# Optimization experiments

Measured on AMD Instinct MI355X. Metric: run time of the kernel, lower is better.

The kernel has to match this reference:

```python
import jax, jax.numpy as jnp
import numpy as np

DK, DV, NH = 512, 256, 8  # matches init_kwargs


def rel_to_abs(x):
    # x: (B, N, L, 2L-1) -> (B, N, L, L) via pad/reshape trick
    B, N, L, _ = x.shape
    x = jnp.pad(x, ((0, 0), (0, 0), (0, 0), (0, 1)))          # (B,N,L,2L)
    x = x.reshape(B, N, L * 2 * L)
    x = jnp.pad(x, ((0, 0), (0, 0), (0, L - 1)))
    x = x.reshape(B, N, L + 1, 2 * L - 1)
    return x[:, :, :L, L - 1:]


def relative_logits_1d(q, rel_k):
    # q: (B, nh, A, Wd, dkh); rel_k: (dkh, 2*Wd-1)
    B, nh, A, Wd, _ = q.shape
    rel = jnp.einsum('bnawc,cm->bnawm', q, rel_k)             # (B,nh,A,Wd,2Wd-1)
    rel = rel.reshape(B, nh * A, Wd, 2 * Wd - 1)
    rel = rel_to_abs(rel).reshape(B, nh, A, 1, Wd, Wd)
    return jnp.broadcast_to(rel, (B, nh, A, A, Wd, Wd))


def reference(x, w_qkv, w_conv, w_out, key_rel_h, key_rel_w):
    B, Cin, H, W = x.shape
    dkh, dvh = DK // NH, DV // NH
    L = H * W
    # 1x1 qkv projection (stride 1)
    qkv = jnp.einsum('bchw,oc->bohw', x, w_qkv)               # (B, 2dk+dv, H, W)
    q = qkv[:, :DK]
    k = qkv[:, DK:2 * DK]
    v = qkv[:, 2 * DK:]
    flat_q = q.reshape(B, NH, dkh, L) * (dkh ** -0.5)
    flat_k = k.reshape(B, NH, dkh, L)
    flat_v = v.reshape(B, NH, dvh, L)
    logits = jnp.einsum('bncs,bnct->bnst', flat_q, flat_k)     # (B,nh,L,L)
    # relative position logits (uses the already-scaled q, as in the torch code)
    qr = flat_q.reshape(B, NH, dkh, H, W).transpose(0, 1, 3, 4, 2)  # (B,nh,H,W,dkh)
    w_rel = relative_logits_1d(qr, key_rel_w)                  # (B,nh,H,H,W,W)
    h_rel = relative_logits_1d(qr.transpose(0, 1, 3, 2, 4), key_rel_h)  # (B,nh,W,W,H,H)
    h_rel = h_rel.transpose(0, 1, 2, 4, 3, 5).reshape(B, NH, L, L)
    w_rel = w_rel.transpose(0, 1, 4, 2, 5, 3).reshape(B, NH, L, L)
    logits = logits + h_rel + w_rel
    weights = jax.nn.softmax(logits, axis=-1)
    attn = jnp.einsum('bnst,bnct->bnsc', weights, flat_v)      # (B,nh,L,dvh)
    attn = attn.transpose(0, 1, 3, 2).reshape(B, DV, H, W)
    attn = jnp.einsum('bchw,oc->bohw', attn, w_out)            # 1x1 out_proj
    conv_out = jax.lax.conv_general_dilated(
        x, w_conv, window_strides=(1, 1), padding=[(1, 1), (1, 1)],
        dimension_numbers=('NCHW', 'OIHW', 'NCHW'))            # (B, out_c-dv, H, W)
    return jnp.concatenate([conv_out, attn], axis=1)


def setup_inputs() -> dict:
    key = jax.random.key(0)
    ks = jax.random.split(key, 6)
    H, W, Cin = 32, 32, 256
    return {
        'x': jax.random.normal(ks[0], (8, Cin, H, W), jnp.float32),
        'w_qkv': jax.random.normal(ks[1], (2 * DK + DV, Cin), jnp.float32) * 0.02,
        'w_conv': jax.random.normal(ks[2], (256, Cin, 3, 3), jnp.float32) * 0.02,
        'w_out': jax.random.normal(ks[3], (DV, DV), jnp.float32) * 0.02,
        'key_rel_h': DK ** -0.5 + jax.random.normal(ks[4], (DK // NH, 2 * H - 1), jnp.float32),
        'key_rel_w': DK ** -0.5 + jax.random.normal(ks[5], (DK // NH, 2 * W - 1), jnp.float32),
    }
```

## Files before the change

kernel.cpp:

```cpp
#include <hip/hip_runtime.h>
#include <cstddef>
#include <cstdint>

#define NB 8
#define CIN 256
#define LL 1024
#define DKC 512
#define DVC 256
#define XPSTRIDE 295936

typedef short short8 __attribute__((ext_vector_type(8)));
typedef float f32x4 __attribute__((ext_vector_type(4)));

__device__ __forceinline__ unsigned short f2bf(float f) {
  unsigned int u = __float_as_uint(f);
  u += 0x7fffu + ((u >> 16) & 1u);
  return (unsigned short)(u >> 16);
}
__device__ __forceinline__ float bf2f(unsigned short u) {
  return __uint_as_float(((unsigned int)u) << 16);
}

__global__ __launch_bounds__(256) void prep_all(
    const float* __restrict__ x, const float* __restrict__ wconv,
    const float* __restrict__ wqkv, const float* __restrict__ wout,
    const float* __restrict__ krh, const float* __restrict__ krw,
    unsigned short* __restrict__ xTp, unsigned short* __restrict__ wtap,
    unsigned short* __restrict__ wqbf, unsigned short* __restrict__ woutbf,
    unsigned short* __restrict__ relTh, unsigned short* __restrict__ relTw) {
  __shared__ float tile[64][65];
  const int bx = blockIdx.x;
  const int tid = threadIdx.x;
  if (bx < 128) {
    const int st = bx & 15;
    const int b = bx >> 4;
    const int s0 = st * 64;
    const int h0 = st * 2;
    for (int cc = 0; cc < 4; ++cc) {
      const int c0 = cc * 64;
      {
        const int row = tid >> 2;
        const int j0 = (tid & 3) * 16;
#pragma unroll
        for (int k = 0; k < 4; ++k)
          *(float4*)&tile[row][j0 + k * 4] =
              *(const float4*)(x + ((size_t)(b * CIN + c0 + row)) * LL + s0 + j0 + k * 4);
      }
      __syncthreads();
      {
        const int sl = tid >> 2;
        const int cb = (tid & 3) * 16;
        unsigned short buf[16];
#pragma unroll
        for (int m = 0; m < 16; ++m) buf[m] = f2bf(tile[cb + m][sl]);
        const int hp = h0 + (sl >> 5) + 1;
        const int wp = (sl & 31) + 1;
        unsigned short* dst = xTp + (size_t)b * XPSTRIDE + (hp * 34 + wp) * 256 + c0 + cb;
        *(uint4*)dst = *(uint4*)&buf[0];
        *(uint4*)(dst + 8) = *(uint4*)&buf[8];
      }
      __syncthreads();
    }
  } else if (bx < 1184) {
    const int idx = (bx - 128) * 256 + tid;
    const int b = idx / 33792;
    const int rem = idx - b * 33792;
    const int pos = rem >> 8, c = rem & 255;
    int hp, wp;
    if (pos < 34) { hp = 0; wp = pos; }
    else if (pos < 68) { hp = 33; wp = pos - 34; }
    else if (pos < 100) { hp = pos - 68 + 1; wp = 0; }
    else { hp = pos - 100 + 1; wp = 33; }
    xTp[(size_t)b * XPSTRIDE + (hp * 34 + wp) * 256 + c] = 0;
  } else {
    const int idx = (bx - 1184) * 256 + tid;
    if (idx < 589824) {
      const int tap = idx >> 16;
      const int rem = idx & 65535;
      wtap[idx] = f2bf(wconv[(size_t)rem * 9 + tap]);
    } else if (idx < 917504) {
      const int j = idx - 589824;
      const int o = j >> 8;
      const float sc = (o < DKC) ? 0.125f * 1.44269504088896f : 1.0f;
      wqbf[j] = f2bf(wqkv[j] * sc);
    } else if (idx < 983040) {
      const int j = idx - 917504;
      woutbf[j] = f2bf(wout[j]);
    } else {
      const int j = idx - 983040;
      const int tbl = j >> 12;
      const int rest = j & 4095;
      const int m = rest >> 6, c = rest & 63;
      const float* src = tbl ? krw : krh;
      unsigned short* dst = tbl ? relTw : relTh;
      const float v = (m < 63) ? src[c * 63 + m] : 0.f;
      dst[m * 64 + c] = f2bf(v);
    }
  }
}

__global__ __launch_bounds__(256) void qkv_mfma(
    const unsigned short* __restrict__ xTp, const unsigned short* __restrict__ wqbf,
    unsigned short* __restrict__ qbf, unsigned short* __restrict__ kbf,
    unsigned short* __restrict__ vbf) {
  __shared__ __align__(16) char smem[16640];
  unsigned short* as = (unsigned short*)smem;
  unsigned short* bs = (unsigned short*)(smem + 8192);
  float (*trans)[65] = (float(*)[65])smem;

  const int tid = threadIdx.x;
  const int lane = tid & 63, w = tid >> 6;
  const int n16 = lane & 15, quad = lane >> 4;
  const int ot = blockIdx.x;
  const int st = blockIdx.y;
  const int b = blockIdx.z;
  const int o0 = ot * 64;
  const int s0 = st * 64;
  const int h0 = st * 2;
  const int trow = tid >> 3, ck = tid & 7;

  const unsigned short* xb = xTp + (size_t)b * XPSTRIDE;
  const unsigned short* wt = wqbf + (size_t)o0 * 256;
  const int wpos = (trow & 31) + 1;

  f32x4 acc[4];
#pragma unroll
  for (int nt = 0; nt < 4; ++nt) acc[nt] = (f32x4){0.f, 0.f, 0.f, 0.f};

  uint4 ra0, ra1, rb0, rb1;
  {
    ra0 = *(const uint4*)(wt + (size_t)trow * 256 + ck * 8);
    ra1 = *(const uint4*)(wt + (size_t)(trow + 32) * 256 + ck * 8);
    rb0 = *(const uint4*)(xb + (size_t)((h0 + 1) * 34 + wpos) * 256 + ck * 8);
    rb1 = *(const uint4*)(xb + (size_t)((h0 + 2) * 34 + wpos) * 256 + ck * 8);
  }
#pragma unroll
  for (int kc = 0; kc < 4; ++kc) {
    __syncthreads();
    *(uint4*)&as[trow * 64 + ((ck ^ (trow & 7)) * 8)] = ra0;
    *(uint4*)&as[(trow + 32) * 64 + ((ck ^ (trow & 7)) * 8)] = ra1;
    *(uint4*)&bs[trow * 64 + ((ck ^ (trow & 7)) * 8)] = rb0;
    *(uint4*)&bs[(trow + 32) * 64 + ((ck ^ (trow & 7)) * 8)] = rb1;
    __syncthreads();
    if (kc < 3) {
      const int c0 = (kc + 1) * 64;
      ra0 = *(const uint4*)(wt + (size_t)trow * 256 + c0 + ck * 8);
      ra1 = *(const uint4*)(wt + (size_t)(trow + 32) * 256 + c0 + ck * 8);
      rb0 = *(const uint4*)(xb + (size_t)((h0 + 1) * 34 + wpos) * 256 + c0 + ck * 8);
      rb1 = *(const uint4*)(xb + (size_t)((h0 + 2) * 34 + wpos) * 256 + c0 + ck * 8);
    }
    short8 a0 = *(const short8*)&as[(w * 16 + n16) * 64 + ((quad ^ (n16 & 7)) * 8)];
    short8 a1 = *(const short8*)&as[(w * 16 + n16) * 64 + (((quad + 4) ^ (n16 & 7)) * 8)];
#pragma unroll
    for (int nt = 0; nt < 4; ++nt) {
      short8 b0 = *(const short8*)&bs[(nt * 16 + n16) * 64 + ((quad ^ (n16 & 7)) * 8)];
      short8 b1 = *(const short8*)&bs[(nt * 16 + n16) * 64 + (((quad + 4) ^ (n16 & 7)) * 8)];
      acc[nt] = __builtin_amdgcn_mfma_f32_16x16x32_bf16(a0, b0, acc[nt], 0, 0, 0);
      acc[nt] = __builtin_amdgcn_mfma_f32_16x16x32_bf16(a1, b1, acc[nt], 0, 0, 0);
    }
  }
  __syncthreads();
#pragma unroll
  for (int nt = 0; nt < 4; ++nt)
#pragma unroll
    for (int reg = 0; reg < 4; ++reg)
      trans[w * 16 + quad * 4 + reg][nt * 16 + n16] = acc[nt][reg];
  __syncthreads();
  const int sl = tid >> 2;
  const int cseg = (tid & 3) * 16;
  unsigned short buf[16];
  if (ot < 16) {
#pragma unroll
    for (int m = 0; m < 16; ++m) buf[m] = f2bf(trans[cseg + m][sl]);
    unsigned short* dst;
    int head;
    if (ot < 8) { dst = qbf; head = ot; }
    else { dst = kbf; head = ot - 8; }
    const size_t base = (((size_t)(b * 8 + head)) * LL + s0 + sl) * 64 + cseg;
    *(uint4*)(dst + base) = *(uint4*)&buf[0];
    *(uint4*)(dst + base + 8) = *(uint4*)&buf[8];
  } else {
#pragma unroll
    for (int m = 0; m < 16; ++m) buf[m] = f2bf(trans[sl][cseg + m]);
    unsigned short* dst = vbf + ((size_t)b * DVC + (ot - 16) * 64 + sl) * LL + s0 + cseg;
    *(uint4*)dst = *(uint4*)&buf[0];
    *(uint4*)(dst + 8) = *(uint4*)&buf[8];
  }
}

__global__ __launch_bounds__(256) void conv_mfma(
    const unsigned short* __restrict__ xTp, const unsigned short* __restrict__ wtap,
    float* __restrict__ out) {
  __shared__ __align__(16) unsigned short as[2][64 * 64];
  __shared__ __align__(16) unsigned short bs[2][64 * 64];
  const int tid = threadIdx.x;
  const int lane = tid & 63, w = tid >> 6;
  const int n16 = lane & 15, quad = lane >> 4;
  const int ot = blockIdx.x;
  const int st = blockIdx.y;
  const int b = blockIdx.z;
  const int s0 = st * 64;
  const int h0 = st * 2;
  const int trow = tid >> 3;
  const int ck = tid & 7;

  const unsigned short* xb = xTp + (size_t)b * XPSTRIDE;
  const unsigned short* wbase = wtap + (size_t)(ot * 64) * 256;

  f32x4 acc[4];
#pragma unroll
  for (int nt = 0; nt < 4; ++nt) acc[nt] = (f32x4){0.f, 0.f, 0.f, 0.f};

  uint4 ra0, ra1, rb0, rb1;
  auto loadtile = [&](int it) {
    const int tap = it >> 2;
    const int c0 = (it & 3) * 64;
    const int dh = tap / 3 - 1;
    const int dw = tap - (tap / 3) * 3 - 1;
    const unsigned short* wt = wbase + (size_t)tap * 65536;
    ra0 = *(const uint4*)(wt + (size_t)trow * 256 + c0 + ck * 8);
    ra1 = *(const uint4*)(wt + (size_t)(trow + 32) * 256 + c0 + ck * 8);
    const int wp = (trow & 31) + dw + 1;
    rb0 = *(const uint4*)(xb + (size_t)((h0 + dh + 1) * 34 + wp) * 256 + c0 + ck * 8);
    rb1 = *(const uint4*)(xb + (size_t)((h0 + dh + 2) * 34 + wp) * 256 + c0 + ck * 8);
  };
  auto stage = [&](int bufi) {
    *(uint4*)&as[bufi][trow * 64 + ((ck ^ (trow & 7)) * 8)] = ra0;
    *(uint4*)&as[bufi][(trow + 32) * 64 + ((ck ^ (trow & 7)) * 8)] = ra1;
    *(uint4*)&bs[bufi][trow * 64 + ((ck ^ (trow & 7)) * 8)] = rb0;
    *(uint4*)&bs[bufi][(trow + 32) * 64 + ((ck ^ (trow & 7)) * 8)] = rb1;
  };
  loadtile(0);
  stage(0);
  for (int it = 0; it < 36; ++it) {
    if (it < 35) loadtile(it + 1);
    __syncthreads();
    const unsigned short* ab = as[it & 1];
    const unsigned short* bb = bs[it & 1];
    short8 a0 = *(const short8*)&ab[(w * 16 + n16) * 64 + ((quad ^ (n16 & 7)) * 8)];
    short8 a1 = *(const short8*)&ab[(w * 16 + n16) * 64 + (((quad + 4) ^ (n16 & 7)) * 8)];
#pragma unroll
    for (int nt = 0; nt < 4; ++nt) {
      short8 b0 = *(const short8*)&bb[(nt * 16 + n16) * 64 + ((quad ^ (n16 & 7)) * 8)];
      short8 b1 = *(const short8*)&bb[(nt * 16 + n16) * 64 + (((quad + 4) ^ (n16 & 7)) * 8)];
      acc[nt] = __builtin_amdgcn_mfma_f32_16x16x32_bf16(a0, b0, acc[nt], 0, 0, 0);
      acc[nt] = __builtin_amdgcn_mfma_f32_16x16x32_bf16(a1, b1, acc[nt], 0, 0, 0);
    }
    if (it < 35) stage((it + 1) & 1);
  }
#pragma unroll
  for (int nt = 0; nt < 4; ++nt)
#pragma unroll
    for (int reg = 0; reg < 4; ++reg)
      out[((size_t)b * 512 + ot * 64 + w * 16 + quad * 4 + reg) * LL + s0 + nt * 16 + n16] =
          acc[nt][reg];
}

__global__ __launch_bounds__(256, 4) void attn_kernel(
    const unsigned short* __restrict__ qbf, const unsigned short* __restrict__ kbf,
    const unsigned short* __restrict__ vbf, const unsigned short* __restrict__ relTh,
    const unsigned short* __restrict__ relTw, unsigned short* __restrict__ abf) {
  __shared__ __align__(16) char smem[40832];
  unsigned short* ks = (unsigned short*)smem;
  unsigned short* vs = (unsigned short*)(smem + 16384);
  unsigned short* ps = (unsigned short*)(smem + 24576);
  unsigned short* rwtT = (unsigned short*)(smem + 32768);
  float* obuf = (float*)smem;

  const int tid = threadIdx.x;
  const int lane = tid & 63, w = tid >> 6;
  const int n16 = lane & 15, quad = lane >> 4;
  const int blk = blockIdx.x;
  const int bn = blk & 63, qb = blk >> 6;
  const int n = bn & 7, b = bn >> 3;
  const int s0 = qb * 64;
  const int aa = 2 * qb + (w >> 1);
  const int pb = (w & 1) * 16;

  const unsigned short* qbase = qbf + ((size_t)(b * 8 + n)) * LL * 64;
  const unsigned short* kbase = kbf + ((size_t)(b * 8 + n)) * LL * 64;
  const unsigned short* vbase = vbf + ((size_t)(b * 8 + n)) * 32 * LL;

  const int ck = tid & 7;
  const int trow = tid >> 3;

  uint4 pk0 = *(const uint4*)(kbase + trow * 64 + ck * 8);
  uint4 pk1 = *(const uint4*)(kbase + (trow + 32) * 64 + ck * 8);
  uint4 pv = *(const uint4*)(vbase + (size_t)trow * LL + ck * 8);

  {
    const int sT = (pb + n16) * 32 + aa;
    short8 ra0 = *(const short8*)(qbase + (size_t)sT * 64 + quad * 8);
    short8 ra1 = *(const short8*)(qbase + (size_t)sT * 64 + 32 + quad * 8);
#pragma unroll
    for (int tbl = 0; tbl < 2; ++tbl) {
      const unsigned short* rel = tbl ? relTh : relTw;
      f32x4 acc[4];
#pragma unroll
      for (int mt = 0; mt < 4; ++mt) acc[mt] = (f32x4){0.f, 0.f, 0.f, 0.f};
#pragma unroll
      for (int mt = 0; mt < 4; ++mt) {
        short8 b0 = *(const short8*)(rel + (mt * 16 + n16) * 64 + quad * 8);
        short8 b1 = *(const short8*)(rel + (mt * 16 + n16) * 64 + 32 + quad * 8);
        acc[mt] = __builtin_amdgcn_mfma_f32_16x16x32_bf16(ra0, b0, acc[mt], 0, 0, 0);
        acc[mt] = __builtin_amdgcn_mfma_f32_16x16x32_bf16(ra1, b1, acc[mt], 0, 0, 0);
      }
      if (tbl == 0) {
#pragma unroll
        for (int mt = 0; mt < 4; ++mt)
          if (mt * 16 + n16 < 63)
#pragma unroll
            for (int reg = 0; reg < 4; ++reg)
              rwtT[(mt * 16 + n16) * 64 +
                   ((w * 16 + quad * 4 + reg) ^ ((n16 & 7) * 8))] = f2bf(acc[mt][reg]);
      } else {
#pragma unroll
        for (int mt = 0; mt < 4; ++mt)
#pragma unroll
          for (int reg = 0; reg < 4; ++reg)
            ps[(w * 16 + quad * 4 + reg) * 64 + mt * 16 + n16] = f2bf(acc[mt][reg]);
      }
    }
  }
  short8 qf0 = *(const short8*)(qbase + (size_t)(s0 + w * 16 + n16) * 64 + quad * 8);
  short8 qf1 = *(const short8*)(qbase + (size_t)(s0 + w * 16 + n16) * 64 + 32 + quad * 8);
  {
    *(uint4*)&ks[trow * 64 + ((ck ^ (trow & 7)) * 8)] = pk0;
    *(uint4*)&ks[(trow + 32) * 64 + ((ck ^ (trow & 7)) * 8)] = pk1;
    *(uint4*)&vs[trow * 64 + ((ck ^ (trow & 7)) * 8)] = pv;
  }
  __syncthreads();
  float rhreg[2][4];
#pragma unroll
  for (int tt1 = 0; tt1 < 2; ++tt1)
#pragma unroll
    for (int reg = 0; reg < 4; ++reg) {
      const int iL = quad * 4 + reg;
      rhreg[tt1][reg] = bf2f(ps[(w * 16 + iL) * 64 + tt1 * 16 + n16 + 31 - pb - iL]);
    }

  float lacc[4] = {0.f, 0.f, 0.f, 0.f};
  f32x4 oacc[2];
  oacc[0] = (f32x4){0.f, 0.f, 0.f, 0.f};
  oacc[1] = (f32x4){0.f, 0.f, 0.f, 0.f};

  unsigned short* psw = ps + w * 1024;
  const int rb = w * 16 + quad * 4;

  int cur = 0;
  for (int kt64 = 0; kt64 < 16; ++kt64) {
    const int t0 = kt64 * 64;
    if (kt64 < 15) {
      const unsigned short* kg = kbase + (size_t)(t0 + 64) * 64;
      pk0 = *(const uint4*)(kg + trow * 64 + ck * 8);
      pk1 = *(const uint4*)(kg + (trow + 32) * 64 + ck * 8);
      pv = *(const uint4*)(vbase + (size_t)trow * LL + t0 + 64 + ck * 8);
    }
    __syncthreads();
    const unsigned short* ksb = ks + cur * 4096;
    const unsigned short* vsb = vs + cur * 2048;

    f32x4 sacc[4];
#pragma unroll
    for (int tt = 0; tt < 4; ++tt) sacc[tt] = (f32x4){0.f, 0.f, 0.f, 0.f};
#pragma unroll
    for (int tt = 0; tt < 4; ++tt) {
      short8 kb0 = *(const short8*)&ksb[(tt * 16 + n16) * 64 + ((quad ^ (n16 & 7)) * 8)];
      short8 kb1 = *(const short8*)&ksb[(tt * 16 + n16) * 64 + (((quad + 4) ^ (n16 & 7)) * 8)];
      sacc[tt] = __builtin_amdgcn_mfma_f32_16x16x32_bf16(qf0, kb0, sacc[tt], 0, 0, 0);
      sacc[tt] = __builtin_amdgcn_mfma_f32_16x16x32_bf16(qf1, kb1, sacc[tt], 0, 0, 0);
    }
    float rwv[2][4];
#pragma unroll
    for (int h = 0; h < 2; ++h) {
      const int mw = (t0 >> 5) + h - aa + 31;
      const ushort4 rw4 = *(const ushort4*)&rwtT[mw * 64 + (rb ^ ((mw & 7) * 8))];
      rwv[h][0] = bf2f(rw4.x); rwv[h][1] = bf2f(rw4.y);
      rwv[h][2] = bf2f(rw4.z); rwv[h][3] = bf2f(rw4.w);
    }
#pragma unroll
    for (int tt = 0; tt < 4; ++tt)
#pragma unroll
      for (int reg = 0; reg < 4; ++reg) {
        const float e =
            __builtin_amdgcn_exp2f(sacc[tt][reg] + rwv[tt >> 1][reg] + rhreg[tt & 1][reg]);
        lacc[reg] += e;
        const int r = quad * 4 + reg;
        psw[r * 64 + (((tt * 2 + (n16 >> 3)) ^ (r & 7)) * 8) + (n16 & 7)] =
            (unsigned short)(__float_as_uint(e) >> 16);
      }
    __asm__ volatile("s_waitcnt lgkmcnt(0)" ::: "memory");
#pragma unroll
    for (int kt = 0; kt < 2; ++kt) {
      short8 pa = *(const short8*)&psw[n16 * 64 + (((quad + 4 * kt) ^ (n16 & 7)) * 8)];
#pragma unroll
      for (int ct = 0; ct < 2; ++ct) {
        short8 vb = *(const short8*)&vsb[(ct * 16 + n16) * 64 + (((quad + 4 * kt) ^ (n16 & 7)) * 8)];
        oacc[ct] = __builtin_amdgcn_mfma_f32_16x16x32_bf16(pa, vb, oacc[ct], 0, 0, 0);
      }
    }
    if (kt64 < 15) {
      unsigned short* kd = ks + (cur ^ 1) * 4096;
      unsigned short* vd = vs + (cur ^ 1) * 2048;
      *(uint4*)&kd[trow * 64 + ((ck ^ (trow & 7)) * 8)] = pk0;
      *(uint4*)&kd[(trow + 32) * 64 + ((ck ^ (trow & 7)) * 8)] = pk1;
      *(uint4*)&vd[trow * 64 + ((ck ^ (trow & 7)) * 8)] = pv;
    }
    cur ^= 1;
  }
  float linv[4];
#pragma unroll
  for (int reg = 0; reg < 4; ++reg) {
    float l = lacc[reg];
#pragma unroll
    for (int m = 1; m < 16; m <<= 1) l += __shfl_xor(l, m, 16);
    linv[reg] = 1.0f / l;
  }
  __syncthreads();
#pragma unroll
  for (int ct = 0; ct < 2; ++ct)
#pragma unroll
    for (int reg = 0; reg < 4; ++reg)
      obuf[(w * 16 + quad * 4 + reg) * 33 + ct * 16 + n16] = oacc[ct][reg] * linv[reg];
  __syncthreads();
  {
    const int row = tid >> 2;
    const int cseg = (tid & 3) * 8;
    unsigned short buf8[8];
#pragma unroll
    for (int m = 0; m < 8; ++m) buf8[m] = f2bf(obuf[row * 33 + cseg + m]);
    *(uint4*)(abf + (((size_t)b * LL) + s0 + row) * 256 + n * 32 + cseg) = *(uint4*)&buf8[0];
  }
}

__global__ __launch_bounds__(256) void proj_mfma(
    const unsigned short* __restrict__ abf, const unsigned short* __restrict__ woutbf,
    float* __restrict__ out) {
  __shared__ __align__(16) unsigned short as[64 * 64];
  __shared__ __align__(16) unsigned short bs[64 * 64];
  const int tid = threadIdx.x;
  const int lane = tid & 63, w = tid >> 6;
  const int n16 = lane & 15, quad = lane >> 4;
  const int ot = blockIdx.x;
  const int st = blockIdx.y;
  const int b = blockIdx.z;
  const int o0 = ot * 64;
  const int s0 = st * 64;
  const int trow = tid >> 3, ck = tid & 7;

  const unsigned short* ab = abf + ((size_t)b * LL + s0) * 256;
  const unsigned short* wt = woutbf + (size_t)o0 * 256;

  f32x4 acc[4];
#pragma unroll
  for (int nt = 0; nt < 4; ++nt) acc[nt] = (f32x4){0.f, 0.f, 0.f, 0.f};

  uint4 ra0, ra1, rb0, rb1;
  ra0 = *(const uint4*)(wt + (size_t)trow * 256 + ck * 8);
  ra1 = *(const uint4*)(wt + (size_t)(trow + 32) * 256 + ck * 8);
  rb0 = *(const uint4*)(ab + (size_t)trow * 256 + ck * 8);
  rb1 = *(const uint4*)(ab + (size_t)(trow + 32) * 256 + ck * 8);
#pragma unroll
  for (int kc = 0; kc < 4; ++kc) {
    __syncthreads();
    *(uint4*)&as[trow * 64 + ((ck ^ (trow & 7)) * 8)] = ra0;
    *(uint4*)&as[(trow + 32) * 64 + ((ck ^ (trow & 7)) * 8)] = ra1;
    *(uint4*)&bs[trow * 64 + ((ck ^ (trow & 7)) * 8)] = rb0;
    *(uint4*)&bs[(trow + 32) * 64 + ((ck ^ (trow & 7)) * 8)] = rb1;
    __syncthreads();
    if (kc < 3) {
      const int c0 = (kc + 1) * 64;
      ra0 = *(const uint4*)(wt + (size_t)trow * 256 + c0 + ck * 8);
      ra1 = *(const uint4*)(wt + (size_t)(trow + 32) * 256 + c0 + ck * 8);
      rb0 = *(const uint4*)(ab + (size_t)trow * 256 + c0 + ck * 8);
      rb1 = *(const uint4*)(ab + (size_t)(trow + 32) * 256 + c0 + ck * 8);
    }
    short8 a0 = *(const short8*)&as[(w * 16 + n16) * 64 + ((quad ^ (n16 & 7)) * 8)];
    short8 a1 = *(const short8*)&as[(w * 16 + n16) * 64 + (((quad + 4) ^ (n16 & 7)) * 8)];
#pragma unroll
    for (int nt = 0; nt < 4; ++nt) {
      short8 b0 = *(const short8*)&bs[(nt * 16 + n16) * 64 + ((quad ^ (n16 & 7)) * 8)];
      short8 b1 = *(const short8*)&bs[(nt * 16 + n16) * 64 + (((quad + 4) ^ (n16 & 7)) * 8)];
      acc[nt] = __builtin_amdgcn_mfma_f32_16x16x32_bf16(a0, b0, acc[nt], 0, 0, 0);
      acc[nt] = __builtin_amdgcn_mfma_f32_16x16x32_bf16(a1, b1, acc[nt], 0, 0, 0);
    }
  }
#pragma unroll
  for (int nt = 0; nt < 4; ++nt)
#pragma unroll
    for (int reg = 0; reg < 4; ++reg)
      out[((size_t)b * 512 + 256 + o0 + w * 16 + quad * 4 + reg) * LL + s0 + nt * 16 + n16] =
          acc[nt][reg];
}

extern "C" void kernel_launch(void* const* d_in, const int* in_sizes, int n_in,
                              void* d_out, int out_size, void* d_ws, size_t ws_size,
                              hipStream_t stream) {
  const float* x     = (const float*)d_in[0];
  const float* wqkv  = (const float*)d_in[1];
  const float* wconv = (const float*)d_in[2];
  const float* wout  = (const float*)d_in[3];
  const float* krh   = (const float*)d_in[4];
  const float* krw   = (const float*)d_in[5];
  float* out = (float*)d_out;

  unsigned short* qbf = (unsigned short*)d_ws;
  unsigned short* kbf = qbf + (size_t)NB * 8 * LL * 64;
  unsigned short* vbf = kbf + (size_t)NB * 8 * LL * 64;
  unsigned short* abf = vbf + (size_t)NB * DVC * LL;
  unsigned short* relTh = abf + (size_t)NB * LL * DVC;
  unsigned short* relTw = relTh + 4096;
  unsigned short* xTp = relTw + 4096;
  unsigned short* wtap = xTp + (size_t)NB * XPSTRIDE;
  unsigned short* wqbf = wtap + 589824;
  unsigned short* woutbf = wqbf + 327680;

  prep_all<<<dim3(5056), 256, 0, stream>>>(x, wconv, wqkv, wout, krh, krw,
                                           xTp, wtap, wqbf, woutbf, relTh, relTw);
  qkv_mfma<<<dim3(20, 16, NB), 256, 0, stream>>>(xTp, wqbf, qbf, kbf, vbf);
  conv_mfma<<<dim3(4, 16, NB), 256, 0, stream>>>(xTp, wtap, out);
  attn_kernel<<<dim3(1024), 256, 0, stream>>>(qbf, kbf, vbf, relTh, relTw, abf);
  proj_mfma<<<dim3(4, 16, NB), 256, 0, stream>>>(abf, woutbf, out);
}
```

Before: 153.3 us.

## Compute transposed QK^T so P stays in registers for the PV MFMA

Swaps the MFMA operand order so each lane holds the score column that matches the A-operand layout of the PV MFMA, and permutes the key rows stored in shared memory to fit. The exp'd probabilities are packed to bf16 with v_cvt_pk_bf16_f32 and fed straight from registers, removing the per-tile shared-memory round trip and its lgkmcnt wait. Shared memory shrinks from 40832 to 32768 bytes by overlaying the rh table on the K buffer region, which needs an extra barrier, and the row-sum reduction becomes two cross-quad shuffles plus a broadcast.

```diff
diff --git a/kernel.cpp b/kernel.cpp
--- a/kernel.cpp
+++ b/kernel.cpp
@@ -260,11 +260,11 @@
     const unsigned short* __restrict__ qbf, const unsigned short* __restrict__ kbf,
     const unsigned short* __restrict__ vbf, const unsigned short* __restrict__ relTh,
     const unsigned short* __restrict__ relTw, unsigned short* __restrict__ abf) {
-  __shared__ __align__(16) char smem[40832];
+  __shared__ __align__(16) char smem[32768];
   unsigned short* ks = (unsigned short*)smem;
   unsigned short* vs = (unsigned short*)(smem + 16384);
-  unsigned short* ps = (unsigned short*)(smem + 24576);
-  unsigned short* rwtT = (unsigned short*)(smem + 32768);
+  unsigned short* rwtT = (unsigned short*)(smem + 24576);
+  unsigned short* ps = (unsigned short*)(smem + 8192);
   float* obuf = (float*)smem;
 
   const int tid = threadIdx.x;
@@ -283,6 +283,11 @@
 
   const int ck = tid & 7;
   const int trow = tid >> 3;
+  const int keyt = (trow & 3) | (((trow >> 3) & 1) << 2);
+  const int krb = (n16 >> 2) * 8 + (n16 & 3);
+  const int kk = (n16 & 3) | (((n16 >> 2) & 1) << 2);
+  const int vk = (n16 & 3) | (((n16 >> 3) & 1) << 2);
+  const int qcol = w * 16 + n16;
 
   uint4 pk0 = *(const uint4*)(kbase + trow * 64 + ck * 8);
   uint4 pk1 = *(const uint4*)(kbase + (trow + 32) * 64 + ck * 8);
@@ -308,11 +313,10 @@
       if (tbl == 0) {
 #pragma unroll
         for (int mt = 0; mt < 4; ++mt)
-          if (mt * 16 + n16 < 63)
-#pragma unroll
-            for (int reg = 0; reg < 4; ++reg)
-              rwtT[(mt * 16 + n16) * 64 +
-                   ((w * 16 + quad * 4 + reg) ^ ((n16 & 7) * 8))] = f2bf(acc[mt][reg]);
+#pragma unroll
+          for (int reg = 0; reg < 4; ++reg)
+            rwtT[(mt * 16 + n16) * 64 +
+                 ((w * 16 + quad * 4 + reg) ^ ((n16 & 7) * 8))] = f2bf(acc[mt][reg]);
       } else {
 #pragma unroll
         for (int mt = 0; mt < 4; ++mt)
@@ -325,27 +329,24 @@
   short8 qf0 = *(const short8*)(qbase + (size_t)(s0 + w * 16 + n16) * 64 + quad * 8);
   short8 qf1 = *(const short8*)(qbase + (size_t)(s0 + w * 16 + n16) * 64 + 32 + quad * 8);
   {
-    *(uint4*)&ks[trow * 64 + ((ck ^ (trow & 7)) * 8)] = pk0;
-    *(uint4*)&ks[(trow + 32) * 64 + ((ck ^ (trow & 7)) * 8)] = pk1;
-    *(uint4*)&vs[trow * 64 + ((ck ^ (trow & 7)) * 8)] = pv;
+    *(uint4*)&ks[trow * 64 + ((ck ^ keyt) * 8)] = pk0;
+    *(uint4*)&ks[(trow + 32) * 64 + ((ck ^ keyt) * 8)] = pk1;
+    *(uint4*)&vs[trow * 64 + ((ck ^ keyt) * 8)] = pv;
   }
   __syncthreads();
   float rhreg[2][4];
 #pragma unroll
-  for (int tt1 = 0; tt1 < 2; ++tt1)
-#pragma unroll
-    for (int reg = 0; reg < 4; ++reg) {
-      const int iL = quad * 4 + reg;
-      rhreg[tt1][reg] = bf2f(ps[(w * 16 + iL) * 64 + tt1 * 16 + n16 + 31 - pb - iL]);
-    }
+  for (int c1 = 0; c1 < 2; ++c1)
+#pragma unroll
+    for (int reg = 0; reg < 4; ++reg)
+      rhreg[c1][reg] =
+          bf2f(ps[qcol * 64 + quad * 8 + c1 * 4 + reg + 31 - pb - n16]);
+  __syncthreads();
 
   float lacc[4] = {0.f, 0.f, 0.f, 0.f};
   f32x4 oacc[2];
   oacc[0] = (f32x4){0.f, 0.f, 0.f, 0.f};
   oacc[1] = (f32x4){0.f, 0.f, 0.f, 0.f};
-
-  unsigned short* psw = ps + w * 1024;
-  const int rb = w * 16 + quad * 4;
 
   int cur = 0;
   for (int kt64 = 0; kt64 < 16; ++kt64) {
@@ -362,60 +363,64 @@
 
     f32x4 sacc[4];
 #pragma unroll
-    for (int tt = 0; tt < 4; ++tt) sacc[tt] = (f32x4){0.f, 0.f, 0.f, 0.f};
-#pragma unroll
-    for (int tt = 0; tt < 4; ++tt) {
-      short8 kb0 = *(const short8*)&ksb[(tt * 16 + n16) * 64 + ((quad ^ (n16 & 7)) * 8)];
-      short8 kb1 = *(const short8*)&ksb[(tt * 16 + n16) * 64 + (((quad + 4) ^ (n16 & 7)) * 8)];
-      sacc[tt] = __builtin_amdgcn_mfma_f32_16x16x32_bf16(qf0, kb0, sacc[tt], 0, 0, 0);
-      sacc[tt] = __builtin_amdgcn_mfma_f32_16x16x32_bf16(qf1, kb1, sacc[tt], 0, 0, 0);
-    }
-    float rwv[2][4];
+    for (int c = 0; c < 4; ++c) sacc[c] = (f32x4){0.f, 0.f, 0.f, 0.f};
+#pragma unroll
+    for (int c = 0; c < 4; ++c) {
+      const int ro = (krb + (c & 1) * 4 + (c >> 1) * 32) * 64;
+      short8 kb0 = *(const short8*)&ksb[ro + ((quad ^ kk) * 8)];
+      short8 kb1 = *(const short8*)&ksb[ro + (((quad + 4) ^ kk) * 8)];
+      sacc[c] = __builtin_amdgcn_mfma_f32_16x16x32_bf16(kb0, qf0, sacc[c], 0, 0, 0);
+      sacc[c] = __builtin_amdgcn_mfma_f32_16x16x32_bf16(kb1, qf1, sacc[c], 0, 0, 0);
+    }
+    float rww[2];
 #pragma unroll
     for (int h = 0; h < 2; ++h) {
       const int mw = (t0 >> 5) + h - aa + 31;
-      const ushort4 rw4 = *(const ushort4*)&rwtT[mw * 64 + (rb ^ ((mw & 7) * 8))];
-      rwv[h][0] = bf2f(rw4.x); rwv[h][1] = bf2f(rw4.y);
-      rwv[h][2] = bf2f(rw4.z); rwv[h][3] = bf2f(rw4.w);
-    }
-#pragma unroll
-    for (int tt = 0; tt < 4; ++tt)
+      rww[h] = bf2f(rwtT[mw * 64 + (qcol ^ ((mw & 7) * 8))]);
+    }
+    unsigned int pkw[2][4];
+#pragma unroll
+    for (int c = 0; c < 4; ++c) {
+      float e[4];
 #pragma unroll
       for (int reg = 0; reg < 4; ++reg) {
-        const float e =
-            __builtin_amdgcn_exp2f(sacc[tt][reg] + rwv[tt >> 1][reg] + rhreg[tt & 1][reg]);
-        lacc[reg] += e;
-        const int r = quad * 4 + reg;
-        psw[r * 64 + (((tt * 2 + (n16 >> 3)) ^ (r & 7)) * 8) + (n16 & 7)] =
-            (unsigned short)(__float_as_uint(e) >> 16);
+        e[reg] = __builtin_amdgcn_exp2f(sacc[c][reg] + rww[c >> 1] + rhreg[c & 1][reg]);
+        lacc[reg] += e[reg];
       }
-    __asm__ volatile("s_waitcnt lgkmcnt(0)" ::: "memory");
+      unsigned int p0, p1;
+      asm("v_cvt_pk_bf16_f32 %0, %1, %2" : "=v"(p0) : "v"(e[0]), "v"(e[1]));
+      asm("v_cvt_pk_bf16_f32 %0, %1, %2" : "=v"(p1) : "v"(e[2]), "v"(e[3]));
+      pkw[c >> 1][(c & 1) * 2] = p0;
+      pkw[c >> 1][(c & 1) * 2 + 1] = p1;
+    }
 #pragma unroll
     for (int kt = 0; kt < 2; ++kt) {
-      short8 pa = *(const short8*)&psw[n16 * 64 + (((quad + 4 * kt) ^ (n16 & 7)) * 8)];
+      uint4 pw;
+      pw.x = pkw[kt][0]; pw.y = pkw[kt][1]; pw.z = pkw[kt][2]; pw.w = pkw[kt][3];
+      short8 pa = *(short8*)&pw;
 #pragma unroll
       for (int ct = 0; ct < 2; ++ct) {
-        short8 vb = *(const short8*)&vsb[(ct * 16 + n16) * 64 + (((quad + 4 * kt) ^ (n16 & 7)) * 8)];
+        short8 vb = *(const short8*)&vsb[(ct * 16 + n16) * 64 + (((quad + 4 * kt) ^ vk) * 8)];
         oacc[ct] = __builtin_amdgcn_mfma_f32_16x16x32_bf16(pa, vb, oacc[ct], 0, 0, 0);
       }
     }
     if (kt64 < 15) {
       unsigned short* kd = ks + (cur ^ 1) * 4096;
       unsigned short* vd = vs + (cur ^ 1) * 2048;
-      *(uint4*)&kd[trow * 64 + ((ck ^ (trow & 7)) * 8)] = pk0;
-      *(uint4*)&kd[(trow + 32) * 64 + ((ck ^ (trow & 7)) * 8)] = pk1;
-      *(uint4*)&vd[trow * 64 + ((ck ^ (trow & 7)) * 8)] = pv;
+      *(uint4*)&kd[trow * 64 + ((ck ^ keyt) * 8)] = pk0;
+      *(uint4*)&kd[(trow + 32) * 64 + ((ck ^ keyt) * 8)] = pk1;
+      *(uint4*)&vd[trow * 64 + ((ck ^ keyt) * 8)] = pv;
     }
     cur ^= 1;
   }
+  float lsum = (lacc[0] + lacc[1]) + (lacc[2] + lacc[3]);
+  lsum += __shfl_xor(lsum, 16);
+  lsum += __shfl_xor(lsum, 32);
+  const float linv_own = 1.0f / lsum;
   float linv[4];
 #pragma unroll
-  for (int reg = 0; reg < 4; ++reg) {
-    float l = lacc[reg];
-#pragma unroll
-    for (int m = 1; m < 16; m <<= 1) l += __shfl_xor(l, m, 16);
-    linv[reg] = 1.0f / l;
-  }
+  for (int reg = 0; reg < 4; ++reg)
+    linv[reg] = __shfl(linv_own, (lane & 48) | (quad * 4 + reg));
   __syncthreads();
 #pragma unroll
   for (int ct = 0; ct < 2; ++ct)
```

Measured after the change: 149.8 us. -2.3%, faster.
